# Kernel tuning notes

Measured on AMD Instinct MI355X. Metric: run time of the kernel, lower is better.

The kernel has to match this reference:

```python
import jax, jax.numpy as jnp
import numpy as np

N, NZ, STATE, HID, H, W = 32, 100, 20, 128, 32, 32
STEPS = 64          # steps_range=(64,64)
NC = 1              # output color channels
THRESH = 0.1        # living-mask threshold


def setup_inputs() -> dict:
    key = jax.random.key(0)
    ks = jax.random.split(key, 11)
    def rn(k, shape, s):
        return jax.random.normal(k, shape, dtype=jnp.float32) * s
    return {
        "z":       jax.random.normal(ks[0], (N, NZ, 1, 1), dtype=jnp.float32),
        "w_init1": rn(ks[1], (50, NZ, 1, 1), 0.1),
        "b_init1": rn(ks[2], (50,), 0.1),
        "w_init2": rn(ks[3], (STATE - 1, 50, 1, 1), 0.1),
        "b_init2": rn(ks[4], (STATE - 1,), 0.1),
        "w_perc":  rn(ks[5], (HID, STATE, 3, 3), 0.1),
        "b_perc":  rn(ks[6], (HID,), 0.1),
        "w_up1":   rn(ks[7], (HID, HID, 1, 1), 0.1),
        "b_up1":   rn(ks[8], (HID,), 0.1),
        "w_up2":   rn(ks[9], (STATE, HID, 1, 1), 0.02),  # torch zero-inits this; small random for nontrivial dynamics
        "b_up2":   rn(ks[10], (STATE,), 0.02),
    }


def _conv(x, w, b, pad):
    y = jax.lax.conv_general_dilated(
        x, w, window_strides=(1, 1), padding=[(pad, pad), (pad, pad)],
        dimension_numbers=("NCHW", "OIHW", "NCHW"))
    return y + b[None, :, None, None]


def _maxpool3(x):
    # MaxPool2d(kernel=3, stride=1, padding=1)
    return jax.lax.reduce_window(
        x, -jnp.inf, jax.lax.max,
        window_dimensions=(1, 1, 3, 3), window_strides=(1, 1, 1, 1),
        padding=[(0, 0), (0, 0), (1, 1), (1, 1)])


def _forward(z, w_init1, b_init1, w_init2, b_init2,
             w_perc, b_perc, w_up1, b_up1, w_up2, b_up2):
    n = z.shape[0]
    # init_state: 1x1 conv -> relu -> 1x1 conv, gives [n, STATE-1, 1, 1]
    init_hidden = _conv(jax.nn.relu(_conv(z, w_init1, b_init1, 0)), w_init2, b_init2, 0)
    cH, cW = H // 2, W // 2
    state = jnp.zeros((n, STATE, H, W), dtype=jnp.float32)
    state = state.at[:, 1:, cH, cW].set(init_hidden[:, :, 0, 0])
    state = state.at[:, 0, cH, cW].set(0.5)

    def step(s, _):
        pre = _maxpool3(s[:, 0:1]) > THRESH          # pre living mask
        perc = _conv(s, w_perc, b_perc, 1)           # 3x3 perceive
        upd = _conv(jax.nn.relu(_conv(perc, w_up1, b_up1, 0)), w_up2, b_up2, 0)
        # stochastic_update with p=1: rand(...) < 1 is always True -> plain add
        s = s + upd
        post = _maxpool3(s[:, 0:1]) > THRESH         # post living mask
        s = s * (pre & post)
        return s, None

    state, _ = jax.lax.scan(step, state, None, length=STEPS)
    return state[:, :NC]


def reference(z, w_init1, b_init1, w_init2, b_init2,
              w_perc, b_perc, w_up1, b_up1, w_up2, b_up2):
    return _forward(z, w_init1, b_init1, w_init2, b_init2,
                    w_perc, b_perc, w_up1, b_up1, w_up2, b_up2)
```

## Files before the change

### kernel.cpp

```cpp
#include <hip/hip_runtime.h>

#define NB 32
#define NZ 100
#define ST 20
#define HID 128
#define HW 32
#define PIX 1024
#define STEPS 64
#define TH 0.1f
#define SCL 0.0625f
#define ISCL 16.0f
#define CPAD 24

typedef _Float16 half8  __attribute__((ext_vector_type(8)));
typedef _Float16 half4v __attribute__((ext_vector_type(4)));
typedef float    floatx4 __attribute__((ext_vector_type(4)));

#define NKS1 7
#define PK 136

__global__ __launch_bounds__(64) void init_state_kernel(
    const float* __restrict__ z, const float* __restrict__ w1,
    const float* __restrict__ b1, const float* __restrict__ w2,
    const float* __restrict__ b2, _Float16* __restrict__ Bh,
    _Float16* __restrict__ Bl, unsigned char* __restrict__ M)
{
    __shared__ float zs[NZ];
    __shared__ float h1[50];
    const int n = blockIdx.x;
    const int t = threadIdx.x;
    for (int i = t; i < NZ; i += 64) zs[i] = z[n * NZ + i];
    __syncthreads();
    if (t < 50) {
        float a = b1[t];
        for (int i = 0; i < NZ; ++i) a += w1[t * NZ + i] * zs[i];
        h1[t] = fmaxf(a, 0.f);
    }
    __syncthreads();
    const int gp = 16 * HW + 16;
    if (t < ST - 1) {
        float a = b2[t];
        for (int j = 0; j < 50; ++j) a += w2[t * 50 + j] * h1[j];
        float vs = a * SCL;
        _Float16 hi = (_Float16)vs;
        Bh[(size_t)n * PIX * CPAD + gp * CPAD + (t + 1)] = hi;
        Bl[(size_t)n * PIX * CPAD + gp * CPAD + (t + 1)] = (_Float16)(vs - (float)hi);
    }
    if (t == 63) {
        Bh[(size_t)n * PIX * CPAD + gp * CPAD] = (_Float16)(0.5f * SCL);
        Bl[(size_t)n * PIX * CPAD + gp * CPAD] = (_Float16)0.f;
    }
    for (int i = t; i < PIX; i += 64) M[n * PIX + i] = 1;
}

__global__ __launch_bounds__(256) void repack_kernel(
    const float* __restrict__ Wp, const float* __restrict__ W1,
    const float* __restrict__ W2,
    _Float16* __restrict__ WpRh, _Float16* __restrict__ WpRl,
    _Float16* __restrict__ W1Rh, _Float16* __restrict__ W1Rl,
    _Float16* __restrict__ W2Rh, _Float16* __restrict__ W2Rl)
{
    int e = blockIdx.x * 256 + threadIdx.x;
    if (e < 28672) {
        int j = e & 7, lane = (e >> 3) & 63, t2 = e >> 9;
        int ks = t2 % 7, w = t2 / 7;
        int m = w * 16 + (lane & 15);
        int k = ks * 32 + ((lane >> 4) << 3) + j;
        int q = k / 24, c = k - q * 24;
        float v = (q < 9 && c < ST) ? Wp[m * 180 + c * 9 + q] : 0.f;
        _Float16 hi = (_Float16)v;
        WpRh[e] = hi; WpRl[e] = (_Float16)(v - (float)hi);
    } else if (e < 45056) {
        int e2 = e - 28672;
        int j = e2 & 7, lane = (e2 >> 3) & 63, t2 = e2 >> 9;
        int ks = t2 & 3, w = t2 >> 2;
        int m = w * 16 + (lane & 15);
        int k = ks * 32 + ((lane >> 4) << 3) + j;
        float v = W1[m * 128 + k];
        _Float16 hi = (_Float16)v;
        W1Rh[e2] = hi; W1Rl[e2] = (_Float16)(v - (float)hi);
    } else if (e < 49152) {
        int e3 = e - 45056;
        int j = e3 & 7, lane = (e3 >> 3) & 63, t2 = e3 >> 9;
        int ks = t2 & 3, mt = t2 >> 2;
        int m = mt * 16 + (lane & 15);
        int k = ks * 32 + ((lane >> 4) << 3) + j;
        float v = (m < ST) ? W2[m * 128 + k] : 0.f;
        _Float16 hi = (_Float16)v;
        W2Rh[e3] = hi; W2Rl[e3] = (_Float16)(v - (float)hi);
    }
}

__global__ __launch_bounds__(128) void u0_kernel(
    const float* __restrict__ bp, const float* __restrict__ W1,
    const float* __restrict__ b1, const float* __restrict__ W2,
    const float* __restrict__ b2,
    _Float16* __restrict__ u0h, _Float16* __restrict__ u0l)
{
    __shared__ float h[128];
    const int t = threadIdx.x;
    float a = b1[t];
    for (int i = 0; i < HID; ++i) a += W1[t * HID + i] * bp[i];
    h[t] = fmaxf(a, 0.f);
    __syncthreads();
    if (t < CPAD) {
        float u = 0.f;
        if (t < ST) {
            u = b2[t];
            for (int j = 0; j < HID; ++j) u += W2[t * HID + j] * h[j];
        }
        float us = u * SCL;
        _Float16 hi = (_Float16)us;
        u0h[t] = hi;
        u0l[t] = (_Float16)(us - (float)hi);
    }
}

__global__ __launch_bounds__(512, 4) void ca_step_kernel(
    const _Float16* __restrict__ Bnh, const _Float16* __restrict__ Bnl,
    const unsigned char* __restrict__ Min,
    _Float16* __restrict__ Boh, _Float16* __restrict__ Bol,
    unsigned char* __restrict__ Mout,
    const _Float16* __restrict__ WpRh, const _Float16* __restrict__ WpRl,
    const float* __restrict__ bp,
    const _Float16* __restrict__ W1Rh, const _Float16* __restrict__ W1Rl,
    const float* __restrict__ b1,
    const _Float16* __restrict__ W2Rh, const _Float16* __restrict__ W2Rl,
    const float* __restrict__ b2,
    const _Float16* __restrict__ u0h, const _Float16* __restrict__ u0l)
{
    __shared__ float bch0[216];
    __shared__ float m4[136];
    __shared__ __align__(16) _Float16 tTh[4 * 34 * 24];
    __shared__ __align__(16) _Float16 tTl[4 * 34 * 24];
    __shared__ __align__(16) _Float16 zero16[8];
    __shared__ __align__(16) _Float16 pH[64 * PK];
    __shared__ __align__(16) _Float16 pL[64 * PK];

    const int n = blockIdx.x;
    const int strip = blockIdx.y;
    const int tid = threadIdx.x;
    const int r0 = strip * 2;
    const size_t nbase = (size_t)n * PIX * CPAD;
    const _Float16* Bh = Bnh + nbase;
    const _Float16* Bl = Bnl + nbase;

    const int wv = __builtin_amdgcn_readfirstlane(tid >> 6);
    const int lane = tid & 63;
    const int col = lane & 15;
    const int quad = lane >> 4;
    const int wm = wv >> 1;
    const int wn = wv & 1;

    if (tid < 216) {
        int r = tid / 36, cq = tid % 36;
        int row = r0 - 2 + r, colg = cq - 2;
        float v = 0.f;
        if (row >= 0 && row < HW && colg >= 0 && colg < HW) {
            int gp = row * HW + colg;
            v = ((float)Bh[gp * CPAD] + (float)Bl[gp * CPAD]) * ISCL;
        }
        bch0[tid] = v;
    }
    unsigned char minb = 0;
    if (tid < 136) {
        int tr = tid / 34, tc = tid % 34;
        int y = r0 - 1 + tr, xc = tc - 1;
        if (y >= 0 && y < HW && xc >= 0 && xc < HW)
            minb = Min[n * PIX + y * HW + xc];
    }
    const int px_s = tid / 3, part = tid % 3;
    half8 gh = {}, gl = {};
    if (tid < 408) {
        int tr = px_s / 34, tc = px_s % 34;
        int y = r0 - 1 + tr, xc = tc - 1;
        if (y >= 0 && y < HW && xc >= 0 && xc < HW) {
            int off = (y * HW + xc) * CPAD + part * 8;
            gh = *(const half8*)(Bh + off);
            gl = *(const half8*)(Bl + off);
        }
    }
    if (tid < 8) zero16[tid] = (_Float16)0.f;
    __syncthreads();

    int alive = 0;
    if (tid < 136) {
        int tr = tid / 34, tc = tid % 34;
        float m = 0.f;
        if (minb) {
            float mx = -1e30f;
            #pragma unroll
            for (int dy = 0; dy < 3; ++dy)
                #pragma unroll
                for (int dx = 0; dx < 3; ++dx)
                    mx = fmaxf(mx, bch0[(tr + dy) * 36 + tc + dx]);
            if (mx > TH) m = 1.f;
        }
        m4[tid] = m;
        alive = (m != 0.f);
    }
    const int any = __syncthreads_or(alive);

    _Float16* BoH = Boh + nbase;
    _Float16* BoL = Bol + nbase;

    if (!any) {
        if (tid < 64)
            Mout[n * PIX + (r0 + (tid >> 5)) * HW + (tid & 31)] = 0;
        if (tid < 192) {
            int pl = tid / 3, pt = tid % 3;
            int gp = (r0 + (pl >> 5)) * HW + (pl & 31);
            *(half8*)(BoH + gp * CPAD + pt * 8) = *(const half8*)(u0h + pt * 8);
            *(half8*)(BoL + gp * CPAD + pt * 8) = *(const half8*)(u0l + pt * 8);
        }
        return;
    }

    if (tid < 408) {
        _Float16 mh = (_Float16)m4[px_s];
        *(half8*)&tTh[px_s * 24 + part * 8] = gh * mh;
        *(half8*)&tTl[px_s * 24 + part * 8] = gl * mh;
    }
    if (tid < 64) {
        int ry = lane >> 5, xx = lane & 31;
        float mx = -1e30f;
        #pragma unroll
        for (int dy = 0; dy < 3; ++dy)
            #pragma unroll
            for (int dx = 0; dx < 3; ++dx)
                mx = fmaxf(mx, bch0[(ry + dy + 1) * 36 + (xx + dx + 1)] *
                               m4[(ry + dy) * 34 + (xx + dx)]);
        Mout[n * PIX + (r0 + ry) * HW + xx] = (mx > TH) ? 1 : 0;
    }
    __syncthreads();

    int koff[NKS1];
    #pragma unroll
    for (int ks = 0; ks < NKS1; ++ks) {
        int k0 = ks * 32 + quad * 8;
        int q = k0 / 24, c0 = k0 - q * 24;
        int dy = q / 3, dx = q - dy * 3;
        koff[ks] = (q < 9) ? (dy * 34 + dx) * 24 + c0 : -1;
    }
    int pbase[2];
    #pragma unroll
    for (int j = 0; j < 2; ++j) {
        int px = (wn * 2 + j) * 16 + col;
        pbase[j] = ((px >> 5) * 34 + (px & 31)) * 24;
    }

    floatx4 acc1[2][2];
    #pragma unroll
    for (int i = 0; i < 2; ++i) {
        floatx4 b = *(const floatx4*)(bp + (wm * 2 + i) * 16 + quad * 4) * SCL;
        acc1[i][0] = b; acc1[i][1] = b;
    }
    #pragma unroll
    for (int ks = 0; ks < NKS1; ++ks) {
        half8 Ah[2], Al[2];
        #pragma unroll
        for (int i = 0; i < 2; ++i) {
            int mt = wm * 2 + i;
            Ah[i] = *(const half8*)(WpRh + ((mt * 7 + ks) * 64 + lane) * 8);
            Al[i] = *(const half8*)(WpRl + ((mt * 7 + ks) * 64 + lane) * 8);
        }
        half8 bh[2], bl[2];
        #pragma unroll
        for (int j = 0; j < 2; ++j) {
            const _Float16* sh = (koff[ks] >= 0) ? (tTh + pbase[j] + koff[ks]) : zero16;
            const _Float16* sl = (koff[ks] >= 0) ? (tTl + pbase[j] + koff[ks]) : zero16;
            bh[j] = *(const half8*)sh;
            bl[j] = *(const half8*)sl;
        }
        #pragma unroll
        for (int i = 0; i < 2; ++i)
            #pragma unroll
            for (int j = 0; j < 2; ++j) {
                acc1[i][j] = __builtin_amdgcn_mfma_f32_16x16x32_f16(Ah[i], bh[j], acc1[i][j], 0, 0, 0);
                acc1[i][j] = __builtin_amdgcn_mfma_f32_16x16x32_f16(Ah[i], bl[j], acc1[i][j], 0, 0, 0);
                acc1[i][j] = __builtin_amdgcn_mfma_f32_16x16x32_f16(Al[i], bh[j], acc1[i][j], 0, 0, 0);
            }
    }
    #pragma unroll
    for (int i = 0; i < 2; ++i)
        #pragma unroll
        for (int j = 0; j < 2; ++j) {
            const int px = (wn * 2 + j) * 16 + col;
            const int mb = (wm * 2 + i) * 16 + quad * 4;
            _Float16 h[4], l[4];
            #pragma unroll
            for (int r = 0; r < 4; ++r) {
                h[r] = (_Float16)acc1[i][j][r];
                l[r] = (_Float16)(acc1[i][j][r] - (float)h[r]);
            }
            *(half4v*)&pH[px * PK + mb] = (half4v){h[0], h[1], h[2], h[3]};
            *(half4v*)&pL[px * PK + mb] = (half4v){l[0], l[1], l[2], l[3]};
        }
    __syncthreads();

    floatx4 acc2[2][2];
    #pragma unroll
    for (int i = 0; i < 2; ++i) {
        floatx4 b = *(const floatx4*)(b1 + (wm * 2 + i) * 16 + quad * 4) * SCL;
        acc2[i][0] = b; acc2[i][1] = b;
    }
    #pragma unroll
    for (int ks = 0; ks < 4; ++ks) {
        half8 Ah[2], Al[2];
        #pragma unroll
        for (int i = 0; i < 2; ++i) {
            int mt = wm * 2 + i;
            Ah[i] = *(const half8*)(W1Rh + ((mt * 4 + ks) * 64 + lane) * 8);
            Al[i] = *(const half8*)(W1Rl + ((mt * 4 + ks) * 64 + lane) * 8);
        }
        half8 bh[2], bl[2];
        #pragma unroll
        for (int j = 0; j < 2; ++j) {
            const int px = (wn * 2 + j) * 16 + col;
            bh[j] = *(const half8*)&pH[px * PK + ks * 32 + quad * 8];
            bl[j] = *(const half8*)&pL[px * PK + ks * 32 + quad * 8];
        }
        #pragma unroll
        for (int i = 0; i < 2; ++i)
            #pragma unroll
            for (int j = 0; j < 2; ++j) {
                acc2[i][j] = __builtin_amdgcn_mfma_f32_16x16x32_f16(Ah[i], bh[j], acc2[i][j], 0, 0, 0);
                acc2[i][j] = __builtin_amdgcn_mfma_f32_16x16x32_f16(Ah[i], bl[j], acc2[i][j], 0, 0, 0);
                acc2[i][j] = __builtin_amdgcn_mfma_f32_16x16x32_f16(Al[i], bh[j], acc2[i][j], 0, 0, 0);
            }
    }
    __syncthreads();
    #pragma unroll
    for (int i = 0; i < 2; ++i)
        #pragma unroll
        for (int j = 0; j < 2; ++j) {
            const int px = (wn * 2 + j) * 16 + col;
            const int mb = (wm * 2 + i) * 16 + quad * 4;
            _Float16 h[4], l[4];
            #pragma unroll
            for (int r = 0; r < 4; ++r) {
                float hv = fmaxf(acc2[i][j][r], 0.f);
                h[r] = (_Float16)hv;
                l[r] = (_Float16)(hv - (float)h[r]);
            }
            *(half4v*)&pH[px * PK + mb] = (half4v){h[0], h[1], h[2], h[3]};
            *(half4v*)&pL[px * PK + mb] = (half4v){l[0], l[1], l[2], l[3]};
        }
    __syncthreads();

    const int mt3 = wv & 1, ntU = wv >> 1;
    floatx4 accU = {0.f, 0.f, 0.f, 0.f};
    const int pxU = ntU * 16 + col;
    #pragma unroll
    for (int ks = 0; ks < 4; ++ks) {
        half8 ah = *(const half8*)(W2Rh + ((mt3 * 4 + ks) * 64 + lane) * 8);
        half8 al = *(const half8*)(W2Rl + ((mt3 * 4 + ks) * 64 + lane) * 8);
        half8 bh = *(const half8*)&pH[pxU * PK + ks * 32 + quad * 8];
        half8 bl = *(const half8*)&pL[pxU * PK + ks * 32 + quad * 8];
        accU = __builtin_amdgcn_mfma_f32_16x16x32_f16(ah, bh, accU, 0, 0, 0);
        accU = __builtin_amdgcn_mfma_f32_16x16x32_f16(ah, bl, accU, 0, 0, 0);
        accU = __builtin_amdgcn_mfma_f32_16x16x32_f16(al, bh, accU, 0, 0, 0);
    }
    const int py = pxU >> 5, pxx = pxU & 31;
    const float mval = m4[(py + 1) * 34 + pxx + 1];
    const int gp = (r0 + py) * HW + pxx;
    const int m0 = mt3 * 16 + quad * 4;
    if (m0 < ST) {
        half4v oh4 = *(const half4v*)(Bh + gp * CPAD + m0);
        half4v ol4 = *(const half4v*)(Bl + gp * CPAD + m0);
        floatx4 b2v = *(const floatx4*)(b2 + m0);
        _Float16 nh[4], nl[4];
        #pragma unroll
        for (int r = 0; r < 4; ++r) {
            float sOld = ((float)oh4[r] + (float)ol4[r]) * ISCL;
            float out = sOld * mval + ISCL * accU[r] + b2v[r];
            float os = out * SCL;
            nh[r] = (_Float16)os;
            nl[r] = (_Float16)(os - (float)nh[r]);
        }
        *(half4v*)(BoH + gp * CPAD + m0) = (half4v){nh[0], nh[1], nh[2], nh[3]};
        *(half4v*)(BoL + gp * CPAD + m0) = (half4v){nl[0], nl[1], nl[2], nl[3]};
    } else if (m0 == 20) {
        *(half4v*)(BoH + gp * CPAD + 20) = (half4v){0, 0, 0, 0};
        *(half4v*)(BoL + gp * CPAD + 20) = (half4v){0, 0, 0, 0};
    }
}

__global__ __launch_bounds__(256) void finalize_kernel(
    const _Float16* __restrict__ Bh, const _Float16* __restrict__ Bl,
    const unsigned char* __restrict__ M, float* __restrict__ out)
{
    const int n = blockIdx.y;
    const int p = blockIdx.x * 256 + threadIdx.x;
    const int y = p >> 5, x = p & 31;
    const size_t nbase = (size_t)n * PIX * CPAD;
    float m = 0.f;
    if (M[n * PIX + p]) {
        float mx = -1e30f;
        for (int dy = -1; dy <= 1; ++dy) {
            int yy = y + dy; if (yy < 0 || yy >= HW) continue;
            for (int dx = -1; dx <= 1; ++dx) {
                int xx = x + dx; if (xx < 0 || xx >= HW) continue;
                int gp = yy * HW + xx;
                float v = ((float)Bh[nbase + gp * CPAD] +
                           (float)Bl[nbase + gp * CPAD]) * ISCL;
                mx = fmaxf(mx, v);
            }
        }
        if (mx > TH) m = 1.f;
    }
    float s0 = ((float)Bh[nbase + p * CPAD] + (float)Bl[nbase + p * CPAD]) * ISCL;
    out[n * PIX + p] = s0 * m;
}

extern "C" void kernel_launch(void* const* d_in, const int* in_sizes, int n_in,
                              void* d_out, int out_size, void* d_ws, size_t ws_size,
                              hipStream_t stream)
{
    const float* z       = (const float*)d_in[0];
    const float* w_init1 = (const float*)d_in[1];
    const float* b_init1 = (const float*)d_in[2];
    const float* w_init2 = (const float*)d_in[3];
    const float* b_init2 = (const float*)d_in[4];
    const float* w_perc  = (const float*)d_in[5];
    const float* b_perc  = (const float*)d_in[6];
    const float* w_up1   = (const float*)d_in[7];
    const float* b_up1   = (const float*)d_in[8];
    const float* w_up2   = (const float*)d_in[9];
    const float* b_up2   = (const float*)d_in[10];

    const size_t SB = (size_t)NB * PIX * CPAD;
    _Float16* B0h = (_Float16*)d_ws;
    _Float16* B0l = B0h + SB;
    _Float16* B1h = B0l + SB;
    _Float16* B1l = B1h + SB;
    unsigned char* M0 = (unsigned char*)(B1l + SB);
    unsigned char* M1 = M0 + NB * PIX;
    _Float16* WpRh = (_Float16*)(M1 + NB * PIX);
    _Float16* WpRl = WpRh + 28672;
    _Float16* W1Rh = WpRl + 28672;
    _Float16* W1Rl = W1Rh + 16384;
    _Float16* W2Rh = W1Rl + 16384;
    _Float16* W2Rl = W2Rh + 4096;
    _Float16* u0h  = W2Rl + 4096;
    _Float16* u0l  = u0h + CPAD;

    repack_kernel<<<192, 256, 0, stream>>>(w_perc, w_up1, w_up2,
                                           WpRh, WpRl, W1Rh, W1Rl, W2Rh, W2Rl);
    u0_kernel<<<1, 128, 0, stream>>>(b_perc, w_up1, b_up1, w_up2, b_up2, u0h, u0l);
    hipMemsetAsync(B0h, 0, SB * 2 * sizeof(_Float16), stream);
    init_state_kernel<<<NB, 64, 0, stream>>>(z, w_init1, b_init1, w_init2,
                                             b_init2, B0h, B0l, M0);

    for (int s = 0; s < STEPS; ++s) {
        const _Float16* bih = (s & 1) ? B1h : B0h;
        const _Float16* bil = (s & 1) ? B1l : B0l;
        _Float16* boh       = (s & 1) ? B0h : B1h;
        _Float16* bol       = (s & 1) ? B0l : B1l;
        const unsigned char* mi = (s & 1) ? M1 : M0;
        unsigned char* mo       = (s & 1) ? M0 : M1;
        ca_step_kernel<<<dim3(NB, 16), 512, 0, stream>>>(
            bih, bil, mi, boh, bol, mo, WpRh, WpRl, b_perc,
            W1Rh, W1Rl, b_up1, W2Rh, W2Rl, b_up2, u0h, u0l);
    }
    finalize_kernel<<<dim3(4, NB), 256, 0, stream>>>(B0h, B0l, M0, (float*)d_out);
}
```

Before: 665.6 us.

## Process four rows per block to halve halo overhead and grid size

Each step block now covers 4 image rows (128 pixels) instead of 2, so the grid shrinks from 32x16 to 32x8 blocks. Each wave computes 4 pixel tiles per MFMA sweep, which reuses the loaded weight fragments across twice as many pixels and cuts redundant halo loads. LDS moves to dynamic shared memory of about 91 KB and launch bounds drop to 2 blocks per CU. The cost is lower occupancy, more register pressure, and only 256 blocks, which may underfill the GPU. Dead strips can also no longer be skipped at the same fine granularity.

```diff
diff --git a/kernel.cpp b/kernel.cpp
--- a/kernel.cpp
+++ b/kernel.cpp
@@ -18,6 +18,19 @@
 
 #define NKS1 7
 #define PK 136
+
+#define RB 4
+#define TPX 204
+#define OPX 128
+
+#define OFF_BCH0  0
+#define OFF_M4    (OFF_BCH0 + 1152)
+#define OFF_TTH   (OFF_M4 + 832)
+#define OFF_TTL   (OFF_TTH + 9792)
+#define OFF_Z16   (OFF_TTL + 9792)
+#define OFF_PH    (OFF_Z16 + 16)
+#define OFF_PL    (OFF_PH + 34816)
+#define LDS_BYTES (OFF_PL + 34816)
 
 __global__ __launch_bounds__(64) void init_state_kernel(
     const float* __restrict__ z, const float* __restrict__ w1,
@@ -116,7 +129,7 @@
     }
 }
 
-__global__ __launch_bounds__(512, 4) void ca_step_kernel(
+__global__ __launch_bounds__(512, 2) void ca_step_kernel(
     const _Float16* __restrict__ Bnh, const _Float16* __restrict__ Bnl,
     const unsigned char* __restrict__ Min,
     _Float16* __restrict__ Boh, _Float16* __restrict__ Bol,
@@ -129,18 +142,19 @@
     const float* __restrict__ b2,
     const _Float16* __restrict__ u0h, const _Float16* __restrict__ u0l)
 {
-    __shared__ float bch0[216];
-    __shared__ float m4[136];
-    __shared__ __align__(16) _Float16 tTh[4 * 34 * 24];
-    __shared__ __align__(16) _Float16 tTl[4 * 34 * 24];
-    __shared__ __align__(16) _Float16 zero16[8];
-    __shared__ __align__(16) _Float16 pH[64 * PK];
-    __shared__ __align__(16) _Float16 pL[64 * PK];
+    extern __shared__ __align__(16) char smem[];
+    float* bch0 = (float*)(smem + OFF_BCH0);
+    float* m4   = (float*)(smem + OFF_M4);
+    _Float16* tTh = (_Float16*)(smem + OFF_TTH);
+    _Float16* tTl = (_Float16*)(smem + OFF_TTL);
+    _Float16* zero16 = (_Float16*)(smem + OFF_Z16);
+    _Float16* pH = (_Float16*)(smem + OFF_PH);
+    _Float16* pL = (_Float16*)(smem + OFF_PL);
 
     const int n = blockIdx.x;
     const int strip = blockIdx.y;
     const int tid = threadIdx.x;
-    const int r0 = strip * 2;
+    const int r0 = strip * RB;
     const size_t nbase = (size_t)n * PIX * CPAD;
     const _Float16* Bh = Bnh + nbase;
     const _Float16* Bl = Bnl + nbase;
@@ -152,7 +166,7 @@
     const int wm = wv >> 1;
     const int wn = wv & 1;
 
-    if (tid < 216) {
+    if (tid < 288) {
         int r = tid / 36, cq = tid % 36;
         int row = r0 - 2 + r, colg = cq - 2;
         float v = 0.f;
@@ -163,28 +177,33 @@
         bch0[tid] = v;
     }
     unsigned char minb = 0;
-    if (tid < 136) {
+    if (tid < TPX) {
         int tr = tid / 34, tc = tid % 34;
         int y = r0 - 1 + tr, xc = tc - 1;
         if (y >= 0 && y < HW && xc >= 0 && xc < HW)
             minb = Min[n * PIX + y * HW + xc];
     }
-    const int px_s = tid / 3, part = tid % 3;
-    half8 gh = {}, gl = {};
-    if (tid < 408) {
-        int tr = px_s / 34, tc = px_s % 34;
-        int y = r0 - 1 + tr, xc = tc - 1;
-        if (y >= 0 && y < HW && xc >= 0 && xc < HW) {
-            int off = (y * HW + xc) * CPAD + part * 8;
-            gh = *(const half8*)(Bh + off);
-            gl = *(const half8*)(Bl + off);
+    half8 gh[2], gl[2];
+    #pragma unroll
+    for (int it = 0; it < 2; ++it) {
+        int idx = tid + 512 * it;
+        gh[it] = (half8){}; gl[it] = (half8){};
+        if (idx < TPX * 3) {
+            int pxs = idx / 3, part = idx % 3;
+            int tr = pxs / 34, tc = pxs % 34;
+            int y = r0 - 1 + tr, xc = tc - 1;
+            if (y >= 0 && y < HW && xc >= 0 && xc < HW) {
+                int off = (y * HW + xc) * CPAD + part * 8;
+                gh[it] = *(const half8*)(Bh + off);
+                gl[it] = *(const half8*)(Bl + off);
+            }
         }
     }
     if (tid < 8) zero16[tid] = (_Float16)0.f;
     __syncthreads();
 
     int alive = 0;
-    if (tid < 136) {
+    if (tid < TPX) {
         int tr = tid / 34, tc = tid % 34;
         float m = 0.f;
         if (minb) {
@@ -205,9 +224,9 @@
     _Float16* BoL = Bol + nbase;
 
     if (!any) {
-        if (tid < 64)
+        if (tid < OPX)
             Mout[n * PIX + (r0 + (tid >> 5)) * HW + (tid & 31)] = 0;
-        if (tid < 192) {
+        if (tid < OPX * 3) {
             int pl = tid / 3, pt = tid % 3;
             int gp = (r0 + (pl >> 5)) * HW + (pl & 31);
             *(half8*)(BoH + gp * CPAD + pt * 8) = *(const half8*)(u0h + pt * 8);
@@ -216,13 +235,18 @@
         return;
     }
 
-    if (tid < 408) {
-        _Float16 mh = (_Float16)m4[px_s];
-        *(half8*)&tTh[px_s * 24 + part * 8] = gh * mh;
-        *(half8*)&tTl[px_s * 24 + part * 8] = gl * mh;
-    }
-    if (tid < 64) {
-        int ry = lane >> 5, xx = lane & 31;
+    #pragma unroll
+    for (int it = 0; it < 2; ++it) {
+        int idx = tid + 512 * it;
+        if (idx < TPX * 3) {
+            int pxs = idx / 3, part = idx % 3;
+            _Float16 mh = (_Float16)m4[pxs];
+            *(half8*)&tTh[pxs * 24 + part * 8] = gh[it] * mh;
+            *(half8*)&tTl[pxs * 24 + part * 8] = gl[it] * mh;
+        }
+    }
+    if (tid < OPX) {
+        int ry = tid >> 5, xx = tid & 31;
         float mx = -1e30f;
         #pragma unroll
         for (int dy = 0; dy < 3; ++dy)
@@ -242,18 +266,19 @@
         int dy = q / 3, dx = q - dy * 3;
         koff[ks] = (q < 9) ? (dy * 34 + dx) * 24 + c0 : -1;
     }
-    int pbase[2];
-    #pragma unroll
-    for (int j = 0; j < 2; ++j) {
-        int px = (wn * 2 + j) * 16 + col;
+    int pbase[4];
+    #pragma unroll
+    for (int j = 0; j < 4; ++j) {
+        int px = (wn * 4 + j) * 16 + col;
         pbase[j] = ((px >> 5) * 34 + (px & 31)) * 24;
     }
 
-    floatx4 acc1[2][2];
+    floatx4 acc1[2][4];
     #pragma unroll
     for (int i = 0; i < 2; ++i) {
         floatx4 b = *(const floatx4*)(bp + (wm * 2 + i) * 16 + quad * 4) * SCL;
-        acc1[i][0] = b; acc1[i][1] = b;
+        #pragma unroll
+        for (int j = 0; j < 4; ++j) acc1[i][j] = b;
     }
     #pragma unroll
     for (int ks = 0; ks < NKS1; ++ks) {
@@ -264,9 +289,9 @@
             Ah[i] = *(const half8*)(WpRh + ((mt * 7 + ks) * 64 + lane) * 8);
             Al[i] = *(const half8*)(WpRl + ((mt * 7 + ks) * 64 + lane) * 8);
         }
-        half8 bh[2], bl[2];
-        #pragma unroll
-        for (int j = 0; j < 2; ++j) {
+        half8 bh[4], bl[4];
+        #pragma unroll
+        for (int j = 0; j < 4; ++j) {
             const _Float16* sh = (koff[ks] >= 0) ? (tTh + pbase[j] + koff[ks]) : zero16;
             const _Float16* sl = (koff[ks] >= 0) ? (tTl + pbase[j] + koff[ks]) : zero16;
             bh[j] = *(const half8*)sh;
@@ -275,7 +300,7 @@
         #pragma unroll
         for (int i = 0; i < 2; ++i)
             #pragma unroll
-            for (int j = 0; j < 2; ++j) {
+            for (int j = 0; j < 4; ++j) {
                 acc1[i][j] = __builtin_amdgcn_mfma_f32_16x16x32_f16(Ah[i], bh[j], acc1[i][j], 0, 0, 0);
                 acc1[i][j] = __builtin_amdgcn_mfma_f32_16x16x32_f16(Ah[i], bl[j], acc1[i][j], 0, 0, 0);
                 acc1[i][j] = __builtin_amdgcn_mfma_f32_16x16x32_f16(Al[i], bh[j], acc1[i][j], 0, 0, 0);
@@ -284,8 +309,8 @@
     #pragma unroll
     for (int i = 0; i < 2; ++i)
         #pragma unroll
-        for (int j = 0; j < 2; ++j) {
-            const int px = (wn * 2 + j) * 16 + col;
+        for (int j = 0; j < 4; ++j) {
+            const int px = (wn * 4 + j) * 16 + col;
             const int mb = (wm * 2 + i) * 16 + quad * 4;
             _Float16 h[4], l[4];
             #pragma unroll
@@ -298,11 +323,12 @@
         }
     __syncthreads();
 
-    floatx4 acc2[2][2];
+    floatx4 acc2[2][4];
     #pragma unroll
     for (int i = 0; i < 2; ++i) {
         floatx4 b = *(const floatx4*)(b1 + (wm * 2 + i) * 16 + quad * 4) * SCL;
-        acc2[i][0] = b; acc2[i][1] = b;
+        #pragma unroll
+        for (int j = 0; j < 4; ++j) acc2[i][j] = b;
     }
     #pragma unroll
     for (int ks = 0; ks < 4; ++ks) {
@@ -313,17 +339,17 @@
             Ah[i] = *(const half8*)(W1Rh + ((mt * 4 + ks) * 64 + lane) * 8);
             Al[i] = *(const half8*)(W1Rl + ((mt * 4 + ks) * 64 + lane) * 8);
         }
-        half8 bh[2], bl[2];
-        #pragma unroll
-        for (int j = 0; j < 2; ++j) {
-            const int px = (wn * 2 + j) * 16 + col;
+        half8 bh[4], bl[4];
+        #pragma unroll
+        for (int j = 0; j < 4; ++j) {
+            const int px = (wn * 4 + j) * 16 + col;
             bh[j] = *(const half8*)&pH[px * PK + ks * 32 + quad * 8];
             bl[j] = *(const half8*)&pL[px * PK + ks * 32 + quad * 8];
         }
         #pragma unroll
         for (int i = 0; i < 2; ++i)
             #pragma unroll
-            for (int j = 0; j < 2; ++j) {
+            for (int j = 0; j < 4; ++j) {
                 acc2[i][j] = __builtin_amdgcn_mfma_f32_16x16x32_f16(Ah[i], bh[j], acc2[i][j], 0, 0, 0);
                 acc2[i][j] = __builtin_amdgcn_mfma_f32_16x16x32_f16(Ah[i], bl[j], acc2[i][j], 0, 0, 0);
                 acc2[i][j] = __builtin_amdgcn_mfma_f32_16x16x32_f16(Al[i], bh[j], acc2[i][j], 0, 0, 0);
@@ -333,8 +359,8 @@
     #pragma unroll
     for (int i = 0; i < 2; ++i)
         #pragma unroll
-        for (int j = 0; j < 2; ++j) {
-            const int px = (wn * 2 + j) * 16 + col;
+        for (int j = 0; j < 4; ++j) {
+            const int px = (wn * 4 + j) * 16 + col;
             const int mb = (wm * 2 + i) * 16 + quad * 4;
             _Float16 h[4], l[4];
             #pragma unroll
@@ -348,41 +374,50 @@
         }
     __syncthreads();
 
-    const int mt3 = wv & 1, ntU = wv >> 1;
-    floatx4 accU = {0.f, 0.f, 0.f, 0.f};
-    const int pxU = ntU * 16 + col;
+    const int mt3 = wv & 1, ntb = (wv >> 1) * 2;
+    floatx4 accU[2];
+    accU[0] = (floatx4){0.f, 0.f, 0.f, 0.f};
+    accU[1] = (floatx4){0.f, 0.f, 0.f, 0.f};
     #pragma unroll
     for (int ks = 0; ks < 4; ++ks) {
         half8 ah = *(const half8*)(W2Rh + ((mt3 * 4 + ks) * 64 + lane) * 8);
         half8 al = *(const half8*)(W2Rl + ((mt3 * 4 + ks) * 64 + lane) * 8);
-        half8 bh = *(const half8*)&pH[pxU * PK + ks * 32 + quad * 8];
-        half8 bl = *(const half8*)&pL[pxU * PK + ks * 32 + quad * 8];
-        accU = __builtin_amdgcn_mfma_f32_16x16x32_f16(ah, bh, accU, 0, 0, 0);
-        accU = __builtin_amdgcn_mfma_f32_16x16x32_f16(ah, bl, accU, 0, 0, 0);
-        accU = __builtin_amdgcn_mfma_f32_16x16x32_f16(al, bh, accU, 0, 0, 0);
-    }
-    const int py = pxU >> 5, pxx = pxU & 31;
-    const float mval = m4[(py + 1) * 34 + pxx + 1];
-    const int gp = (r0 + py) * HW + pxx;
+        #pragma unroll
+        for (int j = 0; j < 2; ++j) {
+            const int pxU = (ntb + j) * 16 + col;
+            half8 bh = *(const half8*)&pH[pxU * PK + ks * 32 + quad * 8];
+            half8 bl = *(const half8*)&pL[pxU * PK + ks * 32 + quad * 8];
+            accU[j] = __builtin_amdgcn_mfma_f32_16x16x32_f16(ah, bh, accU[j], 0, 0, 0);
+            accU[j] = __builtin_amdgcn_mfma_f32_16x16x32_f16(ah, bl, accU[j], 0, 0, 0);
+            accU[j] = __builtin_amdgcn_mfma_f32_16x16x32_f16(al, bh, accU[j], 0, 0, 0);
+        }
+    }
     const int m0 = mt3 * 16 + quad * 4;
-    if (m0 < ST) {
-        half4v oh4 = *(const half4v*)(Bh + gp * CPAD + m0);
-        half4v ol4 = *(const half4v*)(Bl + gp * CPAD + m0);
-        floatx4 b2v = *(const floatx4*)(b2 + m0);
-        _Float16 nh[4], nl[4];
-        #pragma unroll
-        for (int r = 0; r < 4; ++r) {
-            float sOld = ((float)oh4[r] + (float)ol4[r]) * ISCL;
-            float out = sOld * mval + ISCL * accU[r] + b2v[r];
-            float os = out * SCL;
-            nh[r] = (_Float16)os;
-            nl[r] = (_Float16)(os - (float)nh[r]);
-        }
-        *(half4v*)(BoH + gp * CPAD + m0) = (half4v){nh[0], nh[1], nh[2], nh[3]};
-        *(half4v*)(BoL + gp * CPAD + m0) = (half4v){nl[0], nl[1], nl[2], nl[3]};
-    } else if (m0 == 20) {
-        *(half4v*)(BoH + gp * CPAD + 20) = (half4v){0, 0, 0, 0};
-        *(half4v*)(BoL + gp * CPAD + 20) = (half4v){0, 0, 0, 0};
+    #pragma unroll
+    for (int j = 0; j < 2; ++j) {
+        const int pxU = (ntb + j) * 16 + col;
+        const int py = pxU >> 5, pxx = pxU & 31;
+        const float mval = m4[(py + 1) * 34 + pxx + 1];
+        const int gp = (r0 + py) * HW + pxx;
+        if (m0 < ST) {
+            half4v oh4 = *(const half4v*)(Bh + gp * CPAD + m0);
+            half4v ol4 = *(const half4v*)(Bl + gp * CPAD + m0);
+            floatx4 b2v = *(const floatx4*)(b2 + m0);
+            _Float16 nh[4], nl[4];
+            #pragma unroll
+            for (int r = 0; r < 4; ++r) {
+                float sOld = ((float)oh4[r] + (float)ol4[r]) * ISCL;
+                float out = sOld * mval + ISCL * accU[j][r] + b2v[r];
+                float os = out * SCL;
+                nh[r] = (_Float16)os;
+                nl[r] = (_Float16)(os - (float)nh[r]);
+            }
+            *(half4v*)(BoH + gp * CPAD + m0) = (half4v){nh[0], nh[1], nh[2], nh[3]};
+            *(half4v*)(BoL + gp * CPAD + m0) = (half4v){nl[0], nl[1], nl[2], nl[3]};
+        } else if (m0 == 20) {
+            *(half4v*)(BoH + gp * CPAD + 20) = (half4v){0, 0, 0, 0};
+            *(half4v*)(BoL + gp * CPAD + 20) = (half4v){0, 0, 0, 0};
+        }
     }
 }
 
@@ -445,6 +480,9 @@
     _Float16* u0h  = W2Rl + 4096;
     _Float16* u0l  = u0h + CPAD;
 
+    hipFuncSetAttribute((const void*)ca_step_kernel,
+                        hipFuncAttributeMaxDynamicSharedMemorySize, LDS_BYTES);
+
     repack_kernel<<<192, 256, 0, stream>>>(w_perc, w_up1, w_up2,
                                            WpRh, WpRl, W1Rh, W1Rl, W2Rh, W2Rl);
     u0_kernel<<<1, 128, 0, stream>>>(b_perc, w_up1, b_up1, w_up2, b_up2, u0h, u0l);
@@ -459,7 +497,7 @@
         _Float16* bol       = (s & 1) ? B0l : B1l;
         const unsigned char* mi = (s & 1) ? M1 : M0;
         unsigned char* mo       = (s & 1) ? M0 : M1;
-        ca_step_kernel<<<dim3(NB, 16), 512, 0, stream>>>(
+        ca_step_kernel<<<dim3(NB, 8), 512, LDS_BYTES, stream>>>(
             bih, bil, mi, boh, bol, mo, WpRh, WpRl, b_perc,
             W1Rh, W1Rl, b_up1, W2Rh, W2Rl, b_up2, u0h, u0l);
     }
```

Result: slower. 929.7 us (+39.7%).
